# Kernel tuning notes

Measured on AMD Instinct MI355X. Metric: run time of the kernel, lower is better.

## Reference

```python
import jax, jax.numpy as jnp
import numpy as np

T, B, I, D = 512, 64, 512, 1024

def setup_inputs() -> dict:
    key = jax.random.key(0)
    ks = jax.random.split(key, 5)
    s = 0.05  # small init scale to keep gates out of saturation
    return {
        "state_below": jax.random.normal(ks[0], (T, B, I), jnp.float32),
        "mask": jnp.ones((T, B), jnp.float32),
        "W":  jax.random.normal(ks[1], (I, 2 * D), jnp.float32) * s,
        "bW": jnp.zeros((2 * D,), jnp.float32),
        "Wx": jax.random.normal(ks[2], (I, D), jnp.float32) * s,
        "bWx": jnp.zeros((D,), jnp.float32),
        "U":  jax.random.normal(ks[3], (D, 2 * D), jnp.float32) * s,
        "Ux": jax.random.normal(ks[4], (D, D), jnp.float32) * s,
    }

def reference(state_below, mask, W, bW, Wx, bWx, U, Ux):
    dim = Ux.shape[1]
    # Precompute input projections for all timesteps (matches state_below_/state_belowx)
    x_all = state_below @ W + bW       # [T, B, 2D]
    xx_all = state_below @ Wx + bWx    # [T, B, D]

    def step(h, inp):
        m, x_, xx_ = inp               # [B], [B,2D], [B,D]
        preact = h @ U + x_            # [B, 2D]
        r = jax.nn.sigmoid(preact[:, :dim])
        u = jax.nn.sigmoid(preact[:, dim:])
        h_cand = jnp.tanh((h @ Ux) * r + xx_)
        h_new = u * h + (1.0 - u) * h_cand
        h_new = m[:, None] * h_new + (1.0 - m)[:, None] * h
        return h_new, h_new

    h0 = jnp.zeros((state_below.shape[1], dim), state_below.dtype)
    _, result = jax.lax.scan(step, h0, (mask, x_all, xx_all))
    return result  # [T, B, D]
```

## Files before the change

kernel.cpp:

```cpp
#include <hip/hip_runtime.h>
#include <math.h>

#define T_STEPS 512
#define BATCH   64
#define IDIM    512
#define DDIM    1024
#define KH      1024
#define KX      512
#define KT      1536
#define NBLK    256

typedef unsigned short ushort_t;
typedef unsigned long long ull_t;
typedef __attribute__((ext_vector_type(8))) short short8;
typedef __attribute__((ext_vector_type(4))) short short4v;
typedef __attribute__((ext_vector_type(4))) float f32x4;

union U16B { ull_t u[2]; short8 s; };

__device__ __forceinline__ ushort_t f2bf(float f) {
    unsigned int u = __float_as_uint(f);
    u += 0x7fff + ((u >> 16) & 1);
    return (ushort_t)(u >> 16);
}
__device__ __forceinline__ float bf2f(ushort_t s) {
    return __uint_as_float(((unsigned int)s) << 16);
}

__global__ __launch_bounds__(256) void k_build_A(const float* __restrict__ U,
                                                 const float* __restrict__ Ux,
                                                 const float* __restrict__ W,
                                                 const float* __restrict__ Wx,
                                                 ushort_t* __restrict__ Ab) {
    int blk = blockIdx.x;
    int dc = blk / 3, g = blk % 3;
    int tid = threadIdx.x;
    int m = tid & 15, kb = tid >> 4;
    int col = dc * 16 + m;
    size_t rowbase = ((((size_t)dc * 3 + g) * 2 + 0) * 16 + m) * KT;
    for (int k = kb; k < KT; k += 16) {
        float w;
        if (g == 2) {
            w = (k < KH) ? Ux[(size_t)k * DDIM + col]
                         : Wx[(size_t)(k - KH) * DDIM + col];
        } else {
            int c2 = col + (g == 1 ? DDIM : 0);
            w = (k < KH) ? U[(size_t)k * (2 * DDIM) + c2]
                         : W[(size_t)(k - KH) * (2 * DDIM) + c2];
        }
        ushort_t w1 = f2bf(w);
        ushort_t w2 = f2bf(w - bf2f(w1));
        Ab[rowbase + k] = w1;
        Ab[rowbase + (size_t)16 * KT + k] = w2;
    }
}

__global__ __launch_bounds__(256) void k_build_sbB(const float* __restrict__ sb,
                                                   ushort_t* __restrict__ sbB) {
    int blk = blockIdx.x;
    int t = blk >> 2, bt = blk & 3;
    int tid = threadIdx.x;
    int r = tid >> 4, c = tid & 15;
    const float* src = sb + ((size_t)t * BATCH + bt * 16 + r) * IDIM;
    ushort_t* d1 = sbB + ((((size_t)t * 2 + 0) * 4 + bt) * 16 + r) * KX;
    ushort_t* d2 = sbB + ((((size_t)t * 2 + 1) * 4 + bt) * 16 + r) * KX;
#pragma unroll
    for (int rep = 0; rep < 8; ++rep) {
        int i = c * 4 + rep * 64;
        float4 v = *(const float4*)(src + i);
        ushort_t a0 = f2bf(v.x), a1 = f2bf(v.y), a2 = f2bf(v.z), a3 = f2bf(v.w);
        short4v p1 = {(short)a0, (short)a1, (short)a2, (short)a3};
        *(short4v*)(d1 + i) = p1;
        ushort_t b0 = f2bf(v.x - bf2f(a0)), b1 = f2bf(v.y - bf2f(a1));
        ushort_t b2 = f2bf(v.z - bf2f(a2)), b3 = f2bf(v.w - bf2f(a3));
        short4v p2 = {(short)b0, (short)b1, (short)b2, (short)b3};
        *(short4v*)(d2 + i) = p2;
    }
}

__global__ __launch_bounds__(768, 1) void k_scan(
    const ushort_t* __restrict__ Ab, const ushort_t* __restrict__ sbB,
    const float* __restrict__ mask, const float* __restrict__ bW,
    const float* __restrict__ bWx, ushort_t* __restrict__ hB,
    float* __restrict__ out, int* __restrict__ bar)
{
    __shared__ float red[12 * 3 * 4 * 64];
    __shared__ int lflag;

    int tid  = threadIdx.x;
    int lane = tid & 63;
    int ku   = tid >> 6;
    int bid  = blockIdx.x;
    int xcd  = bid & 7, j = bid >> 3;
    int dc   = xcd * 8 + (j & 7);
    int bq   = j >> 3;

    int m = lane & 15, q = lane >> 4;
    int b_lane = bq * 16 + m;

    bool isH  = (ku < 8);
    int kbase = isH ? ku * 128 : KH + (ku - 8) * 128;
    int gidx  = 384 + xcd * 16;

    short8 A1r[3][4];
#pragma unroll
    for (int g = 0; g < 3; ++g) {
        const ushort_t* a1p =
            Ab + ((((size_t)dc * 3 + g) * 2 + 0) * 16 + m) * KT + kbase;
#pragma unroll
        for (int ks = 0; ks < 4; ++ks)
            A1r[g][ks] = *(const short8*)(a1p + ks * 32 + q * 8);
    }

    int dl = tid >> 4, b16 = tid & 15;
    int ed = dc * 16 + (dl & 15), eb = bq * 16 + b16;
    int l_src = ((dl & 15) >> 2) * 16 + b16;
    int rg = dl & 3;
    float bR = 0.f, bU = 0.f, bX = 0.f, hold = 0.f;
    if (tid < 256) { bR = bW[ed]; bU = bW[DDIM + ed]; bX = bWx[ed]; }

    if (tid == 0) lflag = 0;
    __syncthreads();

    const size_t hP = (size_t)2 * 64 * KH;

    for (int t = 0; t < T_STEPS; ++t) {
        const ushort_t* hBin  = hB + (size_t)(t & 1) * hP;
        ushort_t*       hBout = hB + (size_t)((t + 1) & 1) * hP;

        f32x4 accA[3] = {{0,0,0,0},{0,0,0,0},{0,0,0,0}};
        f32x4 accB[3] = {{0,0,0,0},{0,0,0,0},{0,0,0,0}};

        if (isH) {
            if (t > 0) {
                if (ku == 0) {
                    while (__hip_atomic_load(&bar[gidx], __ATOMIC_RELAXED,
                                             __HIP_MEMORY_SCOPE_AGENT) < t)
                        __builtin_amdgcn_s_sleep(1);
                    if (lane == 0)
                        __hip_atomic_store(&lflag, t, __ATOMIC_RELAXED,
                                           __HIP_MEMORY_SCOPE_WORKGROUP);
                } else {
                    while (__hip_atomic_load(&lflag, __ATOMIC_RELAXED,
                                             __HIP_MEMORY_SCOPE_WORKGROUP) < t)
                        __builtin_amdgcn_s_sleep(1);
                }
                const ushort_t* brow = hBin + (size_t)b_lane * KH + kbase;
#pragma unroll
                for (int ks = 0; ks < 4; ++ks) {
                    int off = ks * 32 + q * 8;
                    U16B x1, x2;
                    x1.u[0] = __hip_atomic_load((ull_t*)(brow + off),
                                                __ATOMIC_RELAXED, __HIP_MEMORY_SCOPE_AGENT);
                    x1.u[1] = __hip_atomic_load((ull_t*)(brow + off) + 1,
                                                __ATOMIC_RELAXED, __HIP_MEMORY_SCOPE_AGENT);
                    x2.u[0] = __hip_atomic_load((ull_t*)(brow + (size_t)64 * KH + off),
                                                __ATOMIC_RELAXED, __HIP_MEMORY_SCOPE_AGENT);
                    x2.u[1] = __hip_atomic_load((ull_t*)(brow + (size_t)64 * KH + off) + 1,
                                                __ATOMIC_RELAXED, __HIP_MEMORY_SCOPE_AGENT);
                    short8 B1 = x1.s, B2 = x2.s;
#pragma unroll
                    for (int g = 0; g < 3; ++g) {
                        f32x4* acc = (ks & 1) ? &accB[g] : &accA[g];
                        *acc = __builtin_amdgcn_mfma_f32_16x16x32_bf16(A1r[g][ks], B2, *acc, 0, 0, 0);
                        *acc = __builtin_amdgcn_mfma_f32_16x16x32_bf16(A1r[g][ks], B1, *acc, 0, 0, 0);
                    }
                }
            }
        } else {
            const ushort_t* brow =
                sbB + (size_t)t * (2 * 64 * KX) + (size_t)b_lane * KX + (kbase - KH);
#pragma unroll
            for (int ks = 0; ks < 4; ++ks) {
                int off = ks * 32 + q * 8;
                short8 B1 = *(const short8*)(brow + off);
                short8 B2 = *(const short8*)(brow + (size_t)64 * KX + off);
#pragma unroll
                for (int g = 0; g < 3; ++g) {
                    f32x4* acc = (ks & 1) ? &accB[g] : &accA[g];
                    *acc = __builtin_amdgcn_mfma_f32_16x16x32_bf16(A1r[g][ks], B2, *acc, 0, 0, 0);
                    *acc = __builtin_amdgcn_mfma_f32_16x16x32_bf16(A1r[g][ks], B1, *acc, 0, 0, 0);
                }
            }
        }

#pragma unroll
        for (int g = 0; g < 3; ++g) {
            f32x4 s = accA[g] + accB[g];
#pragma unroll
            for (int r2 = 0; r2 < 4; ++r2)
                red[((ku * 3 + g) * 4 + r2) * 64 + lane] = s[r2];
        }
        __syncthreads();

        if (tid < 256) {
            float sR = 0.f, sU = 0.f, sHu = 0.f, sXx = 0.f;
#pragma unroll
            for (int k2 = 0; k2 < 12; ++k2) {
                sR += red[((k2 * 3 + 0) * 4 + rg) * 64 + l_src];
                sU += red[((k2 * 3 + 1) * 4 + rg) * 64 + l_src];
                float v2 = red[((k2 * 3 + 2) * 4 + rg) * 64 + l_src];
                if (k2 < 8) sHu += v2; else sXx += v2;
            }
            float mk = mask[(t << 6) + eb];
            float r  = 1.f / (1.f + __expf(-(sR + bR)));
            float u  = 1.f / (1.f + __expf(-(sU + bU)));
            float hc = tanhf(sHu * r + sXx + bX);
            float hnv = u * hold + (1.f - u) * hc;
            hnv = mk * hnv + (1.f - mk) * hold;
            hold = hnv;

            out[(size_t)t * (BATCH * DDIM) + (size_t)eb * DDIM + ed] = hnv;
            ushort_t h1 = f2bf(hnv);
            ushort_t h2 = f2bf(hnv - bf2f(h1));
            __hip_atomic_store(hBout + (size_t)eb * KH + ed, h1,
                               __ATOMIC_RELAXED, __HIP_MEMORY_SCOPE_AGENT);
            __hip_atomic_store(hBout + (size_t)64 * KH + (size_t)eb * KH + ed, h2,
                               __ATOMIC_RELAXED, __HIP_MEMORY_SCOPE_AGENT);
        }

        __syncthreads();

        if (t + 1 < T_STEPS) {
            if (tid == 0)
                __hip_atomic_store(&bar[bid], t + 1, __ATOMIC_RELAXED,
                                   __HIP_MEMORY_SCOPE_AGENT);
            if (bid == 0 && ku == 0) {
                int need = t + 1;
                for (;;) {
                    int v0 = __hip_atomic_load(&bar[lane * 4 + 0], __ATOMIC_RELAXED,
                                               __HIP_MEMORY_SCOPE_AGENT);
                    int v1 = __hip_atomic_load(&bar[lane * 4 + 1], __ATOMIC_RELAXED,
                                               __HIP_MEMORY_SCOPE_AGENT);
                    int v2 = __hip_atomic_load(&bar[lane * 4 + 2], __ATOMIC_RELAXED,
                                               __HIP_MEMORY_SCOPE_AGENT);
                    int v3 = __hip_atomic_load(&bar[lane * 4 + 3], __ATOMIC_RELAXED,
                                               __HIP_MEMORY_SCOPE_AGENT);
                    int mn = min(min(v0, v1), min(v2, v3));
                    if (__all(mn >= need)) break;
                }
                if (lane < 8)
                    __hip_atomic_store(&bar[384 + lane * 16], need, __ATOMIC_RELAXED,
                                       __HIP_MEMORY_SCOPE_AGENT);
            }
        }
    }
}

extern "C" void kernel_launch(void* const* d_in, const int* in_sizes, int n_in,
                              void* d_out, int out_size, void* d_ws, size_t ws_size,
                              hipStream_t stream) {
    const float* sb   = (const float*)d_in[0];
    const float* mask = (const float*)d_in[1];
    const float* W    = (const float*)d_in[2];
    const float* bW   = (const float*)d_in[3];
    const float* Wx   = (const float*)d_in[4];
    const float* bWx  = (const float*)d_in[5];
    const float* U    = (const float*)d_in[6];
    const float* Ux   = (const float*)d_in[7];
    float* out = (float*)d_out;

    ushort_t* Ab  = (ushort_t*)d_ws;
    ushort_t* sbB = Ab + (size_t)2 * 3072 * KT;
    ushort_t* hB  = sbB + (size_t)T_STEPS * 2 * 64 * KX;
    int*      bar = (int*)(hB + (size_t)2 * 2 * 64 * KH);

    (void)hipMemsetAsync(bar, 0, 2048, stream);
    k_build_A<<<dim3(192), 256, 0, stream>>>(U, Ux, W, Wx, Ab);
    k_build_sbB<<<dim3(T_STEPS * 4), 256, 0, stream>>>(sb, sbB);

    const ushort_t* AbC = Ab; const ushort_t* sbBC = sbB;
    void* args[] = {(void*)&AbC, (void*)&sbBC, (void*)&mask, (void*)&bW,
                    (void*)&bWx, (void*)&hB, (void*)&out, (void*)&bar};
    (void)hipLaunchCooperativeKernel((const void*)k_scan, dim3(NBLK), dim3(768),
                                     args, 0, stream);
}
```

Measured before the change: 3.406 ms.

## Replace grid barrier with poison-sentinel polling on per-step hidden-state buffers

Adds a scan kernel that writes each timestep's split-bf16 hidden state to its own buffer. The buffers are pre-filled with a poison byte pattern, and consumers spin on atomic loads until no poison word remains. This replaces the global barrier counter, so each block waits only for the data it needs instead of synchronizing the whole grid. In exchange it needs a large memset of T-step history each call, and it relies on no valid bf16 pair matching the poison pattern. It falls back to the old barrier kernel when the workspace is too small.

```diff
diff --git a/kernel.cpp b/kernel.cpp
--- a/kernel.cpp
+++ b/kernel.cpp
@@ -15,6 +15,8 @@
 typedef __attribute__((ext_vector_type(8))) short short8;
 typedef __attribute__((ext_vector_type(4))) short short4v;
 typedef __attribute__((ext_vector_type(4))) float f32x4;
+
+#define POISON 0x7F7F7F7F7F7F7F7FULL
 
 union U16B { ull_t u[2]; short8 s; };
 
@@ -78,7 +80,145 @@
     }
 }
 
-__global__ __launch_bounds__(768, 1) void k_scan(
+__global__ __launch_bounds__(768, 1) void k_scan_p(
+    const ushort_t* __restrict__ Ab, const ushort_t* __restrict__ sbB,
+    const float* __restrict__ mask, const float* __restrict__ bW,
+    const float* __restrict__ bWx, ushort_t* __restrict__ hAll,
+    float* __restrict__ out)
+{
+    __shared__ float red[12 * 3 * 4 * 64];
+
+    int tid  = threadIdx.x;
+    int lane = tid & 63;
+    int ku   = tid >> 6;
+    int bid  = blockIdx.x;
+    int xcd  = bid & 7, j = bid >> 3;
+    int dc   = xcd * 8 + (j & 7);
+    int bq   = j >> 3;
+
+    int m = lane & 15, q = lane >> 4;
+    int b_lane = bq * 16 + m;
+
+    bool isH  = (ku < 8);
+    int kbase = isH ? ku * 128 : KH + (ku - 8) * 128;
+
+    short8 A1r[3][4];
+#pragma unroll
+    for (int g = 0; g < 3; ++g) {
+        const ushort_t* a1p =
+            Ab + ((((size_t)dc * 3 + g) * 2 + 0) * 16 + m) * KT + kbase;
+#pragma unroll
+        for (int ks = 0; ks < 4; ++ks)
+            A1r[g][ks] = *(const short8*)(a1p + ks * 32 + q * 8);
+    }
+
+    int dl = tid >> 4, b16 = tid & 15;
+    int ed = dc * 16 + (dl & 15), eb = bq * 16 + b16;
+    int l_src = ((dl & 15) >> 2) * 16 + b16;
+    int rg = dl & 3;
+    float bR = 0.f, bU = 0.f, bX = 0.f, hold = 0.f;
+    if (tid < 256) { bR = bW[ed]; bU = bW[DDIM + ed]; bX = bWx[ed]; }
+
+    const size_t hP = (size_t)2 * 64 * KH;
+
+    for (int t = 0; t < T_STEPS; ++t) {
+        ushort_t* hOut = hAll + (size_t)t * hP;
+
+        f32x4 accA[3] = {{0,0,0,0},{0,0,0,0},{0,0,0,0}};
+        f32x4 accB[3] = {{0,0,0,0},{0,0,0,0},{0,0,0,0}};
+
+        if (isH) {
+            if (t > 0) {
+                const ushort_t* hIn = hAll + (size_t)(t - 1) * hP;
+                const ushort_t* brow = hIn + (size_t)b_lane * KH + kbase;
+                U16B x1[4], x2[4];
+                for (;;) {
+                    bool ok = true;
+#pragma unroll
+                    for (int ks = 0; ks < 4; ++ks) {
+                        int off = ks * 32 + q * 8;
+                        const ull_t* p1 = (const ull_t*)(brow + off);
+                        const ull_t* p2 = (const ull_t*)(brow + (size_t)64 * KH + off);
+                        x1[ks].u[0] = __hip_atomic_load(p1, __ATOMIC_RELAXED,
+                                                        __HIP_MEMORY_SCOPE_AGENT);
+                        x1[ks].u[1] = __hip_atomic_load(p1 + 1, __ATOMIC_RELAXED,
+                                                        __HIP_MEMORY_SCOPE_AGENT);
+                        x2[ks].u[0] = __hip_atomic_load(p2, __ATOMIC_RELAXED,
+                                                        __HIP_MEMORY_SCOPE_AGENT);
+                        x2[ks].u[1] = __hip_atomic_load(p2 + 1, __ATOMIC_RELAXED,
+                                                        __HIP_MEMORY_SCOPE_AGENT);
+                        ok = ok && (x1[ks].u[0] != POISON) && (x1[ks].u[1] != POISON)
+                                && (x2[ks].u[0] != POISON) && (x2[ks].u[1] != POISON);
+                    }
+                    if (__all(ok)) break;
+                }
+#pragma unroll
+                for (int ks = 0; ks < 4; ++ks) {
+#pragma unroll
+                    for (int g = 0; g < 3; ++g) {
+                        f32x4* acc = (ks & 1) ? &accB[g] : &accA[g];
+                        *acc = __builtin_amdgcn_mfma_f32_16x16x32_bf16(A1r[g][ks], x2[ks].s, *acc, 0, 0, 0);
+                        *acc = __builtin_amdgcn_mfma_f32_16x16x32_bf16(A1r[g][ks], x1[ks].s, *acc, 0, 0, 0);
+                    }
+                }
+            }
+        } else {
+            const ushort_t* brow =
+                sbB + (size_t)t * (2 * 64 * KX) + (size_t)b_lane * KX + (kbase - KH);
+#pragma unroll
+            for (int ks = 0; ks < 4; ++ks) {
+                int off = ks * 32 + q * 8;
+                short8 B1 = *(const short8*)(brow + off);
+                short8 B2 = *(const short8*)(brow + (size_t)64 * KX + off);
+#pragma unroll
+                for (int g = 0; g < 3; ++g) {
+                    f32x4* acc = (ks & 1) ? &accB[g] : &accA[g];
+                    *acc = __builtin_amdgcn_mfma_f32_16x16x32_bf16(A1r[g][ks], B2, *acc, 0, 0, 0);
+                    *acc = __builtin_amdgcn_mfma_f32_16x16x32_bf16(A1r[g][ks], B1, *acc, 0, 0, 0);
+                }
+            }
+        }
+
+#pragma unroll
+        for (int g = 0; g < 3; ++g) {
+            f32x4 s = accA[g] + accB[g];
+#pragma unroll
+            for (int r2 = 0; r2 < 4; ++r2)
+                red[((ku * 3 + g) * 4 + r2) * 64 + lane] = s[r2];
+        }
+        __syncthreads();
+
+        if (tid < 256) {
+            float sR = 0.f, sU = 0.f, sHu = 0.f, sXx = 0.f;
+#pragma unroll
+            for (int k2 = 0; k2 < 12; ++k2) {
+                sR += red[((k2 * 3 + 0) * 4 + rg) * 64 + l_src];
+                sU += red[((k2 * 3 + 1) * 4 + rg) * 64 + l_src];
+                float v2 = red[((k2 * 3 + 2) * 4 + rg) * 64 + l_src];
+                if (k2 < 8) sHu += v2; else sXx += v2;
+            }
+            float mk = mask[(t << 6) + eb];
+            float r  = 1.f / (1.f + __expf(-(sR + bR)));
+            float u  = 1.f / (1.f + __expf(-(sU + bU)));
+            float hc = tanhf(sHu * r + sXx + bX);
+            float hnv = u * hold + (1.f - u) * hc;
+            hnv = mk * hnv + (1.f - mk) * hold;
+            hold = hnv;
+
+            out[(size_t)t * (BATCH * DDIM) + (size_t)eb * DDIM + ed] = hnv;
+            ushort_t h1 = f2bf(hnv);
+            ushort_t h2 = f2bf(hnv - bf2f(h1));
+            __hip_atomic_store(hOut + (size_t)eb * KH + ed, h1,
+                               __ATOMIC_RELAXED, __HIP_MEMORY_SCOPE_AGENT);
+            __hip_atomic_store(hOut + (size_t)64 * KH + (size_t)eb * KH + ed, h2,
+                               __ATOMIC_RELAXED, __HIP_MEMORY_SCOPE_AGENT);
+        }
+
+        __syncthreads();
+    }
+}
+
+__global__ __launch_bounds__(768, 1) void k_scan_fb(
     const ushort_t* __restrict__ Ab, const ushort_t* __restrict__ sbB,
     const float* __restrict__ mask, const float* __restrict__ bW,
     const float* __restrict__ bWx, ushort_t* __restrict__ hB,
@@ -262,16 +402,30 @@
 
     ushort_t* Ab  = (ushort_t*)d_ws;
     ushort_t* sbB = Ab + (size_t)2 * 3072 * KT;
-    ushort_t* hB  = sbB + (size_t)T_STEPS * 2 * 64 * KX;
-    int*      bar = (int*)(hB + (size_t)2 * 2 * 64 * KH);
-
-    (void)hipMemsetAsync(bar, 0, 2048, stream);
+    ushort_t* tail = sbB + (size_t)T_STEPS * 2 * 64 * KX;
+
+    size_t base_bytes  = (size_t)(tail - (ushort_t*)d_ws) * 2;
+    size_t hall_bytes  = (size_t)T_STEPS * 2 * 64 * KH * 2;
+
     k_build_A<<<dim3(192), 256, 0, stream>>>(U, Ux, W, Wx, Ab);
     k_build_sbB<<<dim3(T_STEPS * 4), 256, 0, stream>>>(sb, sbB);
 
     const ushort_t* AbC = Ab; const ushort_t* sbBC = sbB;
-    void* args[] = {(void*)&AbC, (void*)&sbBC, (void*)&mask, (void*)&bW,
-                    (void*)&bWx, (void*)&hB, (void*)&out, (void*)&bar};
-    (void)hipLaunchCooperativeKernel((const void*)k_scan, dim3(NBLK), dim3(768),
-                                     args, 0, stream);
-}
+
+    if (ws_size >= base_bytes + hall_bytes) {
+        ushort_t* hAll = tail;
+        (void)hipMemsetAsync(hAll, 0x7F, hall_bytes, stream);
+        void* args[] = {(void*)&AbC, (void*)&sbBC, (void*)&mask, (void*)&bW,
+                        (void*)&bWx, (void*)&hAll, (void*)&out};
+        (void)hipLaunchCooperativeKernel((const void*)k_scan_p, dim3(NBLK),
+                                         dim3(768), args, 0, stream);
+    } else {
+        ushort_t* hB  = tail;
+        int*      bar = (int*)(hB + (size_t)2 * 2 * 64 * KH);
+        (void)hipMemsetAsync(bar, 0, 2048, stream);
+        void* args[] = {(void*)&AbC, (void*)&sbBC, (void*)&mask, (void*)&bW,
+                        (void*)&bWx, (void*)&hB, (void*)&out, (void*)&bar};
+        (void)hipLaunchCooperativeKernel((const void*)k_scan_fb, dim3(NBLK),
+                                         dim3(768), args, 0, stream);
+    }
+}
```

New measurement: 5.420 ms. 59.1% more time.
